# Kernel tuning notes

Hardware: AMD Instinct MI355X
Metric: run time of the kernel (lower is better)

Reference implementation:

```python
import jax, jax.numpy as jnp
import numpy as np

N = 50000
E = 800000
IN_CH = 256
HID = 32
HEADS = 4
OUT_CH = 40
NEG_SLOPE = 0.2
BN_EPS = 1e-5


def _gat_conv(x, W, att_src, att_dst, bias, src, dst, num_nodes, concat):
    # x: [N, F_in]; W: [F_in, H*C]; att_src/att_dst: [H, C]
    H, C = att_src.shape
    h = (x @ W).reshape(num_nodes, H, C)            # [N, H, C]
    a_src = (h * att_src[None]).sum(-1)             # [N, H]
    a_dst = (h * att_dst[None]).sum(-1)             # [N, H]
    e = jax.nn.leaky_relu(a_src[src] + a_dst[dst], NEG_SLOPE)  # [Etot, H]
    # segment softmax over incoming edges of each destination node
    m = jax.ops.segment_max(e, dst, num_segments=num_nodes)    # [N, H]
    ex = jnp.exp(e - m[dst])
    s = jax.ops.segment_sum(ex, dst, num_segments=num_nodes)   # [N, H]
    alpha = ex / (s[dst] + 1e-16)                   # [Etot, H]
    out = jax.ops.segment_sum(h[src] * alpha[:, :, None], dst,
                              num_segments=num_nodes)          # [N, H, C]
    out = out.reshape(num_nodes, H * C) if concat else out.mean(axis=1)
    return out + bias


def setup_inputs() -> dict:
    key = jax.random.key(0)
    ks = jax.random.split(key, 12)
    x = jax.random.normal(ks[0], (N, IN_CH), dtype=jnp.float32)
    edge_index = jax.random.randint(ks[1], (2, E), 0, N, dtype=jnp.int64)
    # layer 1: in -> heads*hid, concat
    W1 = jax.random.normal(ks[2], (IN_CH, HEADS * HID), dtype=jnp.float32) * (1.0 / np.sqrt(IN_CH))
    att_src1 = jax.random.normal(ks[3], (HEADS, HID), dtype=jnp.float32) * 0.1
    att_dst1 = jax.random.normal(ks[4], (HEADS, HID), dtype=jnp.float32) * 0.1
    b1 = jnp.zeros((HEADS * HID,), dtype=jnp.float32)
    # batch norm over hidden*heads features
    gamma = jnp.ones((HEADS * HID,), dtype=jnp.float32)
    beta = jnp.zeros((HEADS * HID,), dtype=jnp.float32)
    # layer 2: heads*hid -> out, heads=1, mean (concat=False)
    W2 = jax.random.normal(ks[5], (HEADS * HID, OUT_CH), dtype=jnp.float32) * (1.0 / np.sqrt(HEADS * HID))
    att_src2 = jax.random.normal(ks[6], (1, OUT_CH), dtype=jnp.float32) * 0.1
    att_dst2 = jax.random.normal(ks[7], (1, OUT_CH), dtype=jnp.float32) * 0.1
    b2 = jnp.zeros((OUT_CH,), dtype=jnp.float32)
    return {"x": x, "edge_index": edge_index, "W1": W1, "att_src1": att_src1,
            "att_dst1": att_dst1, "b1": b1, "gamma": gamma, "beta": beta,
            "W2": W2, "att_src2": att_src2, "att_dst2": att_dst2, "b2": b2}


def reference(x, edge_index, W1, att_src1, att_dst1, b1, gamma, beta,
              W2, att_src2, att_dst2, b2):
    num_nodes = x.shape[0]
    loops = jnp.arange(num_nodes, dtype=edge_index.dtype)
    src = jnp.concatenate([edge_index[0], loops])   # add self-loops (PyG default)
    dst = jnp.concatenate([edge_index[1], loops])
    h = _gat_conv(x, W1, att_src1, att_dst1, b1, src, dst, num_nodes, concat=True)
    # BatchNorm over nodes (training-mode batch statistics)
    mu = h.mean(axis=0)
    var = h.var(axis=0)
    h = (h - mu) * jax.lax.rsqrt(var + BN_EPS) * gamma + beta
    h = jax.nn.elu(h)
    out = _gat_conv(h, W2, att_src2, att_dst2, b2, src, dst, num_nodes, concat=False)
    return out
```

## Files before the change

### kernel.cpp

```cpp
#include <hip/hip_runtime.h>

#define NN 50000
#define EE 800000
#define FIN 256
#define F1 128
#define F2 40
#define CAP 48
#define G1B ((NN + 63) / 64)
#define FILLB ((EE + 255) / 256)
#define G1PB 3126
#define G2P0 3125
#define G2P1 ((NN + 63) / 64)
#define LSTR 56

typedef unsigned int u32;
typedef unsigned short u16;
typedef _Float16 h8 __attribute__((ext_vector_type(8)));
typedef float f4 __attribute__((ext_vector_type(4)));

static __device__ __forceinline__ u32 f2bf(float f) {
  u32 u = __float_as_uint(f);
  return (u + 0x7FFFu + ((u >> 16) & 1u)) >> 16;
}
#define BF_LO(u) __uint_as_float((u) << 16)
#define BF_HI(u) __uint_as_float((u) & 0xFFFF0000u)

__global__ __launch_bounds__(256) void g1f_kernel(const float* __restrict__ x,
                                                  const float* __restrict__ W1,
                                                  const float* __restrict__ att_src,
                                                  const float* __restrict__ att_dst,
                                                  u32* __restrict__ h1bf,
                                                  float* __restrict__ a_src,
                                                  float* __restrict__ a_dst,
                                                  const int* __restrict__ ei,
                                                  int* __restrict__ cnt,
                                                  u16* __restrict__ csr) {
  __shared__ __align__(16) _Float16 Alds[64 * LSTR];
  __shared__ __align__(16) _Float16 Blds[128 * LSTR];
  const int t = threadIdx.x;

  if (blockIdx.x >= G1B) {
    int e = (blockIdx.x - G1B) * 256 + t;
    if (e < EE) {
      int src = ei[e];
      int dst = ei[EE + e];
      int p = atomicAdd(cnt + dst, 1);
      if (p < CAP) csr[dst * CAP + p] = (u16)src;
    }
    return;
  }

  const int m0 = blockIdx.x * 64;
  const int l  = t & 63;
  const int w  = t >> 6;
  const int q  = l & 15;
  const int hq = l >> 4;

  const int arow  = t >> 2;
  const int akoff = (t & 3) * 8;
  const int bn    = t & 127;
  const int bkh   = (t >> 7) * 16;

  f4 acc[8] = {};

  float ax[8];
  float bx[16];
  {
    int gr = m0 + arow;
    if (gr < NN) {
      float4 u0 = *(const float4*)(x + (size_t)gr * FIN + akoff);
      float4 u1 = *(const float4*)(x + (size_t)gr * FIN + akoff + 4);
      ax[0] = u0.x; ax[1] = u0.y; ax[2] = u0.z; ax[3] = u0.w;
      ax[4] = u1.x; ax[5] = u1.y; ax[6] = u1.z; ax[7] = u1.w;
    } else {
#pragma unroll
      for (int i = 0; i < 8; ++i) ax[i] = 0.f;
    }
#pragma unroll
    for (int i = 0; i < 16; ++i) bx[i] = W1[(size_t)(bkh + i) * F1 + bn];
  }

  for (int s = 0; s < 8; ++s) {
    __syncthreads();
    {
      h8 av;
#pragma unroll
      for (int i = 0; i < 8; ++i) av[i] = (_Float16)ax[i];
      *(h8*)(Alds + arow * LSTR + akoff) = av;
      h8 bv0, bv1;
#pragma unroll
      for (int i = 0; i < 8; ++i) { bv0[i] = (_Float16)bx[i]; bv1[i] = (_Float16)bx[8 + i]; }
      *(h8*)(Blds + bn * LSTR + bkh) = bv0;
      *(h8*)(Blds + bn * LSTR + bkh + 8) = bv1;
    }
    __syncthreads();
    if (s < 7) {
      int k0 = (s + 1) * 32;
      int gr = m0 + arow;
      if (gr < NN) {
        float4 u0 = *(const float4*)(x + (size_t)gr * FIN + k0 + akoff);
        float4 u1 = *(const float4*)(x + (size_t)gr * FIN + k0 + akoff + 4);
        ax[0] = u0.x; ax[1] = u0.y; ax[2] = u0.z; ax[3] = u0.w;
        ax[4] = u1.x; ax[5] = u1.y; ax[6] = u1.z; ax[7] = u1.w;
      } else {
#pragma unroll
        for (int i = 0; i < 8; ++i) ax[i] = 0.f;
      }
#pragma unroll
      for (int i = 0; i < 16; ++i) bx[i] = W1[(size_t)(k0 + bkh + i) * F1 + bn];
    }
    h8 af = *(const h8*)(Alds + (w * 16 + q) * LSTR + hq * 8);
#pragma unroll
    for (int nf = 0; nf < 8; ++nf) {
      h8 bf = *(const h8*)(Blds + (nf * 16 + q) * LSTR + hq * 8);
      acc[nf] = __builtin_amdgcn_mfma_f32_16x16x32_f16(af, bf, acc[nf], 0, 0, 0);
    }
  }

  u16* h1u = (u16*)h1bf;
#pragma unroll
  for (int nf = 0; nf < 8; ++nf) {
    int ph = nf >> 1;
#pragma unroll
    for (int r = 0; r < 4; ++r) {
      int grow = m0 + w * 16 + hq * 4 + r;
      if (grow < NN)
        h1u[((size_t)ph * NN + grow) * 32 + (nf & 1) * 16 + q] = (u16)f2bf(acc[nf][r]);
    }
  }
  float as8[8], ad8[8];
#pragma unroll
  for (int nf = 0; nf < 8; ++nf) {
    as8[nf] = att_src[nf * 16 + q];
    ad8[nf] = att_dst[nf * 16 + q];
  }
#pragma unroll
  for (int r = 0; r < 4; ++r) {
    float p0 = acc[0][r] * as8[0] + acc[1][r] * as8[1];
    float p1 = acc[2][r] * as8[2] + acc[3][r] * as8[3];
    float p2 = acc[4][r] * as8[4] + acc[5][r] * as8[5];
    float p3 = acc[6][r] * as8[6] + acc[7][r] * as8[7];
    float d0 = acc[0][r] * ad8[0] + acc[1][r] * ad8[1];
    float d1 = acc[2][r] * ad8[2] + acc[3][r] * ad8[3];
    float d2 = acc[4][r] * ad8[4] + acc[5][r] * ad8[5];
    float d3 = acc[6][r] * ad8[6] + acc[7][r] * ad8[7];
#pragma unroll
    for (int off = 1; off < 16; off <<= 1) {
      p0 += __shfl_xor(p0, off); p1 += __shfl_xor(p1, off);
      p2 += __shfl_xor(p2, off); p3 += __shfl_xor(p3, off);
      d0 += __shfl_xor(d0, off); d1 += __shfl_xor(d1, off);
      d2 += __shfl_xor(d2, off); d3 += __shfl_xor(d3, off);
    }
    int grow = m0 + w * 16 + hq * 4 + r;
    if (grow < NN && q < 8) {
      float vs = (q & 2) ? ((q & 1) ? p3 : p2) : ((q & 1) ? p1 : p0);
      float vd = (q & 2) ? ((q & 1) ? d3 : d2) : ((q & 1) ? d1 : d0);
      if (q < 4) a_src[grow * 4 + q] = vs;
      else       a_dst[grow * 4 + (q - 4)] = vd;
    }
  }
}

__global__ __launch_bounds__(256) void gather1_kernel(const int* __restrict__ cnt,
                                                      const u16* __restrict__ csr,
                                                      const float* __restrict__ a_src,
                                                      const float* __restrict__ a_dst,
                                                      const u32* __restrict__ h1bf,
                                                      const float* __restrict__ b1,
                                                      float* __restrict__ h1b,
                                                      float* __restrict__ bnsum,
                                                      float* __restrict__ bnsq) {
  __shared__ float bns[32], bnq[32];
  int t = threadIdx.x;
  if (t < 32) { bns[t] = 0.f; bnq[t] = 0.f; }
  __syncthreads();
  int d = blockIdx.x;
  int xcd = d & 7;
  int p = xcd >> 1;
  int nb = ((d >> 3) << 1) + (xcd & 1);
  int n = nb * 16 + (t >> 4);
  int sub = t & 15;
  int g = sub >> 2;
  int l = sub & 3;
  int f0 = p * 32 + l * 8;
  float acc[8] = {0.f, 0.f, 0.f, 0.f, 0.f, 0.f, 0.f, 0.f};
  float ssum = 0.f;
  if (n < NN) {
    float adst = a_dst[n * 4 + p];
    const u32* hb = h1bf + (size_t)p * NN * 16 + l * 4;
    if (g == 0) {
      float e0 = a_src[n * 4 + p] + adst;
      e0 = e0 > 0.f ? e0 : 0.2f * e0;
      float x0 = __expf(e0);
      uint4 qv = *(const uint4*)(hb + (size_t)n * 16);
      acc[0] = fmaf(x0, BF_LO(qv.x), acc[0]); acc[1] = fmaf(x0, BF_HI(qv.x), acc[1]);
      acc[2] = fmaf(x0, BF_LO(qv.y), acc[2]); acc[3] = fmaf(x0, BF_HI(qv.y), acc[3]);
      acc[4] = fmaf(x0, BF_LO(qv.z), acc[4]); acc[5] = fmaf(x0, BF_HI(qv.z), acc[5]);
      acc[6] = fmaf(x0, BF_LO(qv.w), acc[6]); acc[7] = fmaf(x0, BF_HI(qv.w), acc[7]);
      ssum += x0;
    }
    const u16* row = csr + (size_t)n * CAP;
    int m = cnt[n]; if (m > CAP) m = CAP;
    int i = g;
    for (; i + 4 < m; i += 8) {
      int s0 = row[i];
      int s1 = row[i + 4];
      float e0 = a_src[s0 * 4 + p];
      float e1 = a_src[s1 * 4 + p];
      uint4 q0 = *(const uint4*)(hb + (size_t)s0 * 16);
      uint4 q1 = *(const uint4*)(hb + (size_t)s1 * 16);
      e0 += adst; e0 = e0 > 0.f ? e0 : 0.2f * e0;  float x0 = __expf(e0);
      e1 += adst; e1 = e1 > 0.f ? e1 : 0.2f * e1;  float x1 = __expf(e1);
      acc[0] = fmaf(x0, BF_LO(q0.x), acc[0]); acc[1] = fmaf(x0, BF_HI(q0.x), acc[1]);
      acc[2] = fmaf(x0, BF_LO(q0.y), acc[2]); acc[3] = fmaf(x0, BF_HI(q0.y), acc[3]);
      acc[4] = fmaf(x0, BF_LO(q0.z), acc[4]); acc[5] = fmaf(x0, BF_HI(q0.z), acc[5]);
      acc[6] = fmaf(x0, BF_LO(q0.w), acc[6]); acc[7] = fmaf(x0, BF_HI(q0.w), acc[7]);
      acc[0] = fmaf(x1, BF_LO(q1.x), acc[0]); acc[1] = fmaf(x1, BF_HI(q1.x), acc[1]);
      acc[2] = fmaf(x1, BF_LO(q1.y), acc[2]); acc[3] = fmaf(x1, BF_HI(q1.y), acc[3]);
      acc[4] = fmaf(x1, BF_LO(q1.z), acc[4]); acc[5] = fmaf(x1, BF_HI(q1.z), acc[5]);
      acc[6] = fmaf(x1, BF_LO(q1.w), acc[6]); acc[7] = fmaf(x1, BF_HI(q1.w), acc[7]);
      ssum += x0 + x1;
    }
    for (; i < m; i += 4) {
      int s0 = row[i];
      float e0 = a_src[s0 * 4 + p] + adst;
      e0 = e0 > 0.f ? e0 : 0.2f * e0;
      float x0 = __expf(e0);
      uint4 qv = *(const uint4*)(hb + (size_t)s0 * 16);
      acc[0] = fmaf(x0, BF_LO(qv.x), acc[0]); acc[1] = fmaf(x0, BF_HI(qv.x), acc[1]);
      acc[2] = fmaf(x0, BF_LO(qv.y), acc[2]); acc[3] = fmaf(x0, BF_HI(qv.y), acc[3]);
      acc[4] = fmaf(x0, BF_LO(qv.z), acc[4]); acc[5] = fmaf(x0, BF_HI(qv.z), acc[5]);
      acc[6] = fmaf(x0, BF_LO(qv.w), acc[6]); acc[7] = fmaf(x0, BF_HI(qv.w), acc[7]);
      ssum += x0;
    }
  }
#pragma unroll
  for (int j = 0; j < 8; ++j) {
    acc[j] += __shfl_xor(acc[j], 4);
    acc[j] += __shfl_xor(acc[j], 8);
  }
  ssum += __shfl_xor(ssum, 4);
  ssum += __shfl_xor(ssum, 8);
  if (n < NN && g == 0) {
    float inv = 1.f / (ssum + 1e-16f);
    float4 b0 = *(const float4*)(b1 + f0);
    float4 b4 = *(const float4*)(b1 + f0 + 4);
    float o[8];
    o[0] = acc[0] * inv + b0.x; o[1] = acc[1] * inv + b0.y;
    o[2] = acc[2] * inv + b0.z; o[3] = acc[3] * inv + b0.w;
    o[4] = acc[4] * inv + b4.x; o[5] = acc[5] * inv + b4.y;
    o[6] = acc[6] * inv + b4.z; o[7] = acc[7] * inv + b4.w;
    float4 w0 = {o[0], o[1], o[2], o[3]};
    float4 w1 = {o[4], o[5], o[6], o[7]};
    *(float4*)(h1b + (size_t)n * F1 + f0) = w0;
    *(float4*)(h1b + (size_t)n * F1 + f0 + 4) = w1;
    int lb = l * 8;
#pragma unroll
    for (int j = 0; j < 8; ++j) {
      atomicAdd(&bns[lb + j], o[j]);
      atomicAdd(&bnq[lb + j], o[j] * o[j]);
    }
  }
  __syncthreads();
  if (t < 32) {
    atomicAdd(bnsum + p * 32 + t, bns[t]);
    atomicAdd(bnsq + p * 32 + t, bnq[t]);
  }
}

__global__ __launch_bounds__(256) void gemm2_kernel(const float* __restrict__ hpre,
                                                    const float* __restrict__ W2,
                                                    const float* __restrict__ bnsum,
                                                    const float* __restrict__ bnsq,
                                                    const float* __restrict__ gamma,
                                                    const float* __restrict__ beta,
                                                    u16* __restrict__ h2a,
                                                    u16* __restrict__ h2b,
                                                    const float* __restrict__ att_src2,
                                                    const float* __restrict__ att_dst2,
                                                    float* __restrict__ a_src2,
                                                    float* __restrict__ a_dst2) {
  __shared__ float Wlds[128 * 40];
  __shared__ float Alds[16 * 128];
  __shared__ float sc[128], sh[128];
  int t = threadIdx.x;
  for (int i = t; i < 128 * 40; i += 256) Wlds[i] = W2[i];
  if (t < 128) {
    const float invN = 1.f / (float)NN;
    float mu = bnsum[t] * invN;
    float var = bnsq[t] * invN - mu * mu;
    float s = gamma[t] * rsqrtf(var + 1e-5f);
    sc[t] = s;
    sh[t] = beta[t] - mu * s;
  }
  int tr = t >> 3;
  int tc = t & 7;
  float as5[5], ad5[5];
#pragma unroll
  for (int j = 0; j < 5; ++j) { as5[j] = att_src2[tc * 5 + j]; ad5[j] = att_dst2[tc * 5 + j]; }
  int n0 = blockIdx.x * 128;
  int lrow = t >> 1;
  int lkk = (t & 1) * 8;
  float acc[4][5];
#pragma unroll
  for (int i = 0; i < 4; ++i)
#pragma unroll
    for (int j = 0; j < 5; ++j) acc[i][j] = 0.f;

  for (int k0 = 0; k0 < F1; k0 += 16) {
    float av[8];
    int gn = n0 + lrow;
    if (gn < NN) {
      float4 v0 = *(const float4*)(hpre + (size_t)gn * F1 + k0 + lkk);
      float4 v1 = *(const float4*)(hpre + (size_t)gn * F1 + k0 + lkk + 4);
      av[0] = v0.x; av[1] = v0.y; av[2] = v0.z; av[3] = v0.w;
      av[4] = v1.x; av[5] = v1.y; av[6] = v1.z; av[7] = v1.w;
    } else {
#pragma unroll
      for (int j = 0; j < 8; ++j) av[j] = 0.f;
    }
    __syncthreads();
#pragma unroll
    for (int j = 0; j < 8; ++j) {
      int kg = k0 + lkk + j;
      float a = av[j] * sc[kg] + sh[kg];
      a = a > 0.f ? a : (__expf(a) - 1.f);
      Alds[(lkk + j) * 128 + lrow] = a;
    }
    __syncthreads();
#pragma unroll
    for (int k = 0; k < 16; ++k) {
      float4 a4 = *(const float4*)(Alds + k * 128 + tr * 4);
      float aa[4] = {a4.x, a4.y, a4.z, a4.w};
      float w[5];
#pragma unroll
      for (int j = 0; j < 5; ++j) w[j] = Wlds[(k0 + k) * 40 + tc * 5 + j];
#pragma unroll
      for (int i = 0; i < 4; ++i)
#pragma unroll
        for (int j = 0; j < 5; ++j) acc[i][j] = fmaf(aa[i], w[j], acc[i][j]);
    }
  }
#pragma unroll
  for (int i = 0; i < 4; ++i) {
    int gn = n0 + tr * 4 + i;
    if (gn < NN) {
#pragma unroll
      for (int j = 0; j < 5; ++j) {
        int f = tc * 5 + j;
        u16 v = (u16)f2bf(acc[i][j]);
        if (f < 32) h2a[(size_t)gn * 32 + f] = v;
        else        h2b[(size_t)gn * 8 + (f - 32)] = v;
      }
    }
  }
#pragma unroll
  for (int i = 0; i < 4; ++i) {
    float ps = 0.f, pd = 0.f;
#pragma unroll
    for (int j = 0; j < 5; ++j) { ps += acc[i][j] * as5[j]; pd += acc[i][j] * ad5[j]; }
#pragma unroll
    for (int off = 1; off < 8; off <<= 1) {
      ps += __shfl_xor(ps, off);
      pd += __shfl_xor(pd, off);
    }
    if (tc == 0) {
      int gn = n0 + tr * 4 + i;
      if (gn < NN) { a_src2[gn] = ps; a_dst2[gn] = pd; }
    }
  }
}

__global__ __launch_bounds__(256) void gather2_kernel(const int* __restrict__ cnt,
                                                      const u16* __restrict__ csr,
                                                      const float* __restrict__ a_src,
                                                      const float* __restrict__ a_dst,
                                                      const u32* __restrict__ h2a,
                                                      const u32* __restrict__ h2b,
                                                      const float* __restrict__ b2,
                                                      float* __restrict__ out) {
  int t = threadIdx.x;
  int d = blockIdx.x;
  if (d < G2P0) {
    int n = d * 16 + (t >> 4);
    int sub = t & 15;
    int g = sub >> 2;
    int l = sub & 3;
    float adst = a_dst[n];
    const u32* hb = h2a + l * 4;
    float acc[8] = {0.f, 0.f, 0.f, 0.f, 0.f, 0.f, 0.f, 0.f};
    float ssum = 0.f;
    if (g == 0) {
      float e0 = a_src[n] + adst;
      e0 = e0 > 0.f ? e0 : 0.2f * e0;
      float x0 = __expf(e0);
      uint4 qv = *(const uint4*)(hb + (size_t)n * 16);
      acc[0] = fmaf(x0, BF_LO(qv.x), acc[0]); acc[1] = fmaf(x0, BF_HI(qv.x), acc[1]);
      acc[2] = fmaf(x0, BF_LO(qv.y), acc[2]); acc[3] = fmaf(x0, BF_HI(qv.y), acc[3]);
      acc[4] = fmaf(x0, BF_LO(qv.z), acc[4]); acc[5] = fmaf(x0, BF_HI(qv.z), acc[5]);
      acc[6] = fmaf(x0, BF_LO(qv.w), acc[6]); acc[7] = fmaf(x0, BF_HI(qv.w), acc[7]);
      ssum += x0;
    }
    const u16* row = csr + (size_t)n * CAP;
    int m = cnt[n]; if (m > CAP) m = CAP;
    int i = g;
    for (; i + 4 < m; i += 8) {
      int s0 = row[i];
      int s1 = row[i + 4];
      float e0 = a_src[s0];
      float e1 = a_src[s1];
      uint4 q0 = *(const uint4*)(hb + (size_t)s0 * 16);
      uint4 q1 = *(const uint4*)(hb + (size_t)s1 * 16);
      e0 += adst; e0 = e0 > 0.f ? e0 : 0.2f * e0;  float x0 = __expf(e0);
      e1 += adst; e1 = e1 > 0.f ? e1 : 0.2f * e1;  float x1 = __expf(e1);
      acc[0] = fmaf(x0, BF_LO(q0.x), acc[0]); acc[1] = fmaf(x0, BF_HI(q0.x), acc[1]);
      acc[2] = fmaf(x0, BF_LO(q0.y), acc[2]); acc[3] = fmaf(x0, BF_HI(q0.y), acc[3]);
      acc[4] = fmaf(x0, BF_LO(q0.z), acc[4]); acc[5] = fmaf(x0, BF_HI(q0.z), acc[5]);
      acc[6] = fmaf(x0, BF_LO(q0.w), acc[6]); acc[7] = fmaf(x0, BF_HI(q0.w), acc[7]);
      acc[0] = fmaf(x1, BF_LO(q1.x), acc[0]); acc[1] = fmaf(x1, BF_HI(q1.x), acc[1]);
      acc[2] = fmaf(x1, BF_LO(q1.y), acc[2]); acc[3] = fmaf(x1, BF_HI(q1.y), acc[3]);
      acc[4] = fmaf(x1, BF_LO(q1.z), acc[4]); acc[5] = fmaf(x1, BF_HI(q1.z), acc[5]);
      acc[6] = fmaf(x1, BF_LO(q1.w), acc[6]); acc[7] = fmaf(x1, BF_HI(q1.w), acc[7]);
      ssum += x0 + x1;
    }
    for (; i < m; i += 4) {
      int s0 = row[i];
      float e0 = a_src[s0] + adst;
      e0 = e0 > 0.f ? e0 : 0.2f * e0;
      float x0 = __expf(e0);
      uint4 qv = *(const uint4*)(hb + (size_t)s0 * 16);
      acc[0] = fmaf(x0, BF_LO(qv.x), acc[0]); acc[1] = fmaf(x0, BF_HI(qv.x), acc[1]);
      acc[2] = fmaf(x0, BF_LO(qv.y), acc[2]); acc[3] = fmaf(x0, BF_HI(qv.y), acc[3]);
      acc[4] = fmaf(x0, BF_LO(qv.z), acc[4]); acc[5] = fmaf(x0, BF_HI(qv.z), acc[5]);
      acc[6] = fmaf(x0, BF_LO(qv.w), acc[6]); acc[7] = fmaf(x0, BF_HI(qv.w), acc[7]);
      ssum += x0;
    }
#pragma unroll
    for (int j = 0; j < 8; ++j) {
      acc[j] += __shfl_xor(acc[j], 4);
      acc[j] += __shfl_xor(acc[j], 8);
    }
    ssum += __shfl_xor(ssum, 4);
    ssum += __shfl_xor(ssum, 8);
    if (g == 0) {
      float inv = 1.f / (ssum + 1e-16f);
      int f0 = l * 8;
      float4 b0 = *(const float4*)(b2 + f0);
      float4 b4 = *(const float4*)(b2 + f0 + 4);
      float4 w0 = {acc[0] * inv + b0.x, acc[1] * inv + b0.y,
                   acc[2] * inv + b0.z, acc[3] * inv + b0.w};
      float4 w1 = {acc[4] * inv + b4.x, acc[5] * inv + b4.y,
                   acc[6] * inv + b4.z, acc[7] * inv + b4.w};
      *(float4*)(out + (size_t)n * F2 + f0) = w0;
      *(float4*)(out + (size_t)n * F2 + f0 + 4) = w1;
    }
  } else {
    int n = (d - G2P0) * 64 + (t >> 2);
    int g = t & 3;
    float acc[8] = {0.f, 0.f, 0.f, 0.f, 0.f, 0.f, 0.f, 0.f};
    float ssum = 0.f;
    if (n < NN) {
      float adst = a_dst[n];
      if (g == 0) {
        float e0 = a_src[n] + adst;
        e0 = e0 > 0.f ? e0 : 0.2f * e0;
        float x0 = __expf(e0);
        uint4 qv = *(const uint4*)(h2b + (size_t)n * 4);
        acc[0] = fmaf(x0, BF_LO(qv.x), acc[0]); acc[1] = fmaf(x0, BF_HI(qv.x), acc[1]);
        acc[2] = fmaf(x0, BF_LO(qv.y), acc[2]); acc[3] = fmaf(x0, BF_HI(qv.y), acc[3]);
        acc[4] = fmaf(x0, BF_LO(qv.z), acc[4]); acc[5] = fmaf(x0, BF_HI(qv.z), acc[5]);
        acc[6] = fmaf(x0, BF_LO(qv.w), acc[6]); acc[7] = fmaf(x0, BF_HI(qv.w), acc[7]);
        ssum += x0;
      }
      const u16* row = csr + (size_t)n * CAP;
      int m = cnt[n]; if (m > CAP) m = CAP;
      int i = g;
      for (; i + 4 < m; i += 8) {
        int s0 = row[i];
        int s1 = row[i + 4];
        float e0 = a_src[s0];
        float e1 = a_src[s1];
        uint4 q0 = *(const uint4*)(h2b + (size_t)s0 * 4);
        uint4 q1 = *(const uint4*)(h2b + (size_t)s1 * 4);
        e0 += adst; e0 = e0 > 0.f ? e0 : 0.2f * e0;  float x0 = __expf(e0);
        e1 += adst; e1 = e1 > 0.f ? e1 : 0.2f * e1;  float x1 = __expf(e1);
        acc[0] = fmaf(x0, BF_LO(q0.x), acc[0]); acc[1] = fmaf(x0, BF_HI(q0.x), acc[1]);
        acc[2] = fmaf(x0, BF_LO(q0.y), acc[2]); acc[3] = fmaf(x0, BF_HI(q0.y), acc[3]);
        acc[4] = fmaf(x0, BF_LO(q0.z), acc[4]); acc[5] = fmaf(x0, BF_HI(q0.z), acc[5]);
        acc[6] = fmaf(x0, BF_LO(q0.w), acc[6]); acc[7] = fmaf(x0, BF_HI(q0.w), acc[7]);
        acc[0] = fmaf(x1, BF_LO(q1.x), acc[0]); acc[1] = fmaf(x1, BF_HI(q1.x), acc[1]);
        acc[2] = fmaf(x1, BF_LO(q1.y), acc[2]); acc[3] = fmaf(x1, BF_HI(q1.y), acc[3]);
        acc[4] = fmaf(x1, BF_LO(q1.z), acc[4]); acc[5] = fmaf(x1, BF_HI(q1.z), acc[5]);
        acc[6] = fmaf(x1, BF_LO(q1.w), acc[6]); acc[7] = fmaf(x1, BF_HI(q1.w), acc[7]);
        ssum += x0 + x1;
      }
      for (; i < m; i += 4) {
        int s0 = row[i];
        float e0 = a_src[s0] + adst;
        e0 = e0 > 0.f ? e0 : 0.2f * e0;
        float x0 = __expf(e0);
        uint4 qv = *(const uint4*)(h2b + (size_t)s0 * 4);
        acc[0] = fmaf(x0, BF_LO(qv.x), acc[0]); acc[1] = fmaf(x0, BF_HI(qv.x), acc[1]);
        acc[2] = fmaf(x0, BF_LO(qv.y), acc[2]); acc[3] = fmaf(x0, BF_HI(qv.y), acc[3]);
        acc[4] = fmaf(x0, BF_LO(qv.z), acc[4]); acc[5] = fmaf(x0, BF_HI(qv.z), acc[5]);
        acc[6] = fmaf(x0, BF_LO(qv.w), acc[6]); acc[7] = fmaf(x0, BF_HI(qv.w), acc[7]);
        ssum += x0;
      }
    }
#pragma unroll
    for (int j = 0; j < 8; ++j) {
      acc[j] += __shfl_xor(acc[j], 1);
      acc[j] += __shfl_xor(acc[j], 2);
    }
    ssum += __shfl_xor(ssum, 1);
    ssum += __shfl_xor(ssum, 2);
    if (n < NN && g == 0) {
      float inv = 1.f / (ssum + 1e-16f);
      float4 b0 = *(const float4*)(b2 + 32);
      float4 b4 = *(const float4*)(b2 + 36);
      float4 w0 = {acc[0] * inv + b0.x, acc[1] * inv + b0.y,
                   acc[2] * inv + b0.z, acc[3] * inv + b0.w};
      float4 w1 = {acc[4] * inv + b4.x, acc[5] * inv + b4.y,
                   acc[6] * inv + b4.z, acc[7] * inv + b4.w};
      *(float4*)(out + (size_t)n * F2 + 32) = w0;
      *(float4*)(out + (size_t)n * F2 + 36) = w1;
    }
  }
}

extern "C" void kernel_launch(void* const* d_in, const int* in_sizes, int n_in,
                              void* d_out, int out_size, void* d_ws, size_t ws_size,
                              hipStream_t stream) {
  const float* x        = (const float*)d_in[0];
  const int*   ei       = (const int*)d_in[1];
  const float* W1       = (const float*)d_in[2];
  const float* att_src1 = (const float*)d_in[3];
  const float* att_dst1 = (const float*)d_in[4];
  const float* b1       = (const float*)d_in[5];
  const float* gamma    = (const float*)d_in[6];
  const float* beta     = (const float*)d_in[7];
  const float* W2       = (const float*)d_in[8];
  const float* att_src2 = (const float*)d_in[9];
  const float* att_dst2 = (const float*)d_in[10];
  const float* b2       = (const float*)d_in[11];
  float* out = (float*)d_out;

  int* cnt      = (int*)d_ws;
  float* bnsum  = (float*)(cnt + 50048);
  float* bnsq   = bnsum + 128;
  u16* csr      = (u16*)(bnsq + 128);
  u32* h1bf     = (u32*)(csr + (size_t)NN * CAP);
  float* h1b    = (float*)(h1bf + 3200000);
  u32* h2a      = (u32*)(h1b + 6400000);
  u32* h2b      = h2a + 800000;
  float* a_src1 = (float*)(h2b + 200000);
  float* a_dst1 = a_src1 + 200000;
  float* a_src2 = a_dst1 + 200000;
  float* a_dst2 = a_src2 + 50000;

  hipMemsetAsync(cnt, 0, (50048 + 256) * sizeof(int), stream);

  g1f_kernel<<<G1B + FILLB, 256, 0, stream>>>(x, W1, att_src1, att_dst1,
                                              h1bf, a_src1, a_dst1,
                                              ei, cnt, csr);
  gather1_kernel<<<(G1PB / 2) * 8, 256, 0, stream>>>(cnt, csr, a_src1, a_dst1,
                                                     h1bf, b1, h1b, bnsum, bnsq);
  gemm2_kernel<<<(NN + 127) / 128, 256, 0, stream>>>(h1b, W2, bnsum, bnsq,
                                                     gamma, beta,
                                                     (u16*)h2a, (u16*)h2b,
                                                     att_src2, att_dst2,
                                                     a_src2, a_dst2);
  gather2_kernel<<<G2P0 + G2P1, 256, 0, stream>>>(cnt, csr, a_src2, a_dst2,
                                                  h2a, h2b, b2, out);
}
```

Baseline: 290.2 us.

## Stage CSR rows in LDS and split edges contiguously with shuffled attention loads

```diff
diff --git a/kernel.cpp b/kernel.cpp
--- a/kernel.cpp
+++ b/kernel.cpp
@@ -24,6 +24,12 @@
 }
 #define BF_LO(u) __uint_as_float((u) << 16)
 #define BF_HI(u) __uint_as_float((u) & 0xFFFF0000u)
+
+static __device__ __forceinline__ int sel4i(int a, int b, int c, int d, int k) {
+  int lo = (k & 1) ? b : a;
+  int hi = (k & 1) ? d : c;
+  return (k & 2) ? hi : lo;
+}
 
 __global__ __launch_bounds__(256) void g1f_kernel(const float* __restrict__ x,
                                                   const float* __restrict__ W1,
@@ -171,21 +177,26 @@
                                                       float* __restrict__ bnsum,
                                                       float* __restrict__ bnsq) {
   __shared__ float bns[32], bnq[32];
+  __shared__ __align__(16) u16 idx[16 * CAP];
   int t = threadIdx.x;
   if (t < 32) { bns[t] = 0.f; bnq[t] = 0.f; }
-  __syncthreads();
   int d = blockIdx.x;
   int xcd = d & 7;
   int p = xcd >> 1;
   int nb = ((d >> 3) << 1) + (xcd & 1);
-  int n = nb * 16 + (t >> 4);
+  int base_n = nb * 16;
+  bool blk_ok = (nb < 3125);
+  if (blk_ok && t < 96)
+    ((uint4*)idx)[t] = ((const uint4*)(csr + (size_t)base_n * CAP))[t];
+  __syncthreads();
+  int n = base_n + (t >> 4);
   int sub = t & 15;
   int g = sub >> 2;
   int l = sub & 3;
   int f0 = p * 32 + l * 8;
   float acc[8] = {0.f, 0.f, 0.f, 0.f, 0.f, 0.f, 0.f, 0.f};
   float ssum = 0.f;
-  if (n < NN) {
+  if (blk_ok) {
     float adst = a_dst[n * 4 + p];
     const u32* hb = h1bf + (size_t)p * NN * 16 + l * 4;
     if (g == 0) {
@@ -199,18 +210,30 @@
       acc[6] = fmaf(x0, BF_LO(qv.w), acc[6]); acc[7] = fmaf(x0, BF_HI(qv.w), acc[7]);
       ssum += x0;
     }
-    const u16* row = csr + (size_t)n * CAP;
+    const u16* lrow = idx + (t >> 4) * CAP;
     int m = cnt[n]; if (m > CAP) m = CAP;
-    int i = g;
-    for (; i + 4 < m; i += 8) {
-      int s0 = row[i];
-      int s1 = row[i + 4];
-      float e0 = a_src[s0 * 4 + p];
-      float e1 = a_src[s1 * 4 + p];
+    int sp = (m + 3) >> 2;
+    int i = g * sp;
+    int end = i + sp; if (end > m) end = m;
+    int gb = (t & 63) & ~3;
+    for (; i + 3 < end; i += 4) {
+      int s0 = lrow[i + 0];
+      int s1 = lrow[i + 1];
+      int s2 = lrow[i + 2];
+      int s3 = lrow[i + 3];
+      float av = a_src[sel4i(s0, s1, s2, s3, l) * 4 + p];
       uint4 q0 = *(const uint4*)(hb + (size_t)s0 * 16);
       uint4 q1 = *(const uint4*)(hb + (size_t)s1 * 16);
-      e0 += adst; e0 = e0 > 0.f ? e0 : 0.2f * e0;  float x0 = __expf(e0);
-      e1 += adst; e1 = e1 > 0.f ? e1 : 0.2f * e1;  float x1 = __expf(e1);
+      uint4 q2 = *(const uint4*)(hb + (size_t)s2 * 16);
+      uint4 q3 = *(const uint4*)(hb + (size_t)s3 * 16);
+      float e0 = __shfl(av, gb + 0, 64) + adst;
+      float e1 = __shfl(av, gb + 1, 64) + adst;
+      float e2 = __shfl(av, gb + 2, 64) + adst;
+      float e3 = __shfl(av, gb + 3, 64) + adst;
+      e0 = e0 > 0.f ? e0 : 0.2f * e0;  float x0 = __expf(e0);
+      e1 = e1 > 0.f ? e1 : 0.2f * e1;  float x1 = __expf(e1);
+      e2 = e2 > 0.f ? e2 : 0.2f * e2;  float x2 = __expf(e2);
+      e3 = e3 > 0.f ? e3 : 0.2f * e3;  float x3 = __expf(e3);
       acc[0] = fmaf(x0, BF_LO(q0.x), acc[0]); acc[1] = fmaf(x0, BF_HI(q0.x), acc[1]);
       acc[2] = fmaf(x0, BF_LO(q0.y), acc[2]); acc[3] = fmaf(x0, BF_HI(q0.y), acc[3]);
       acc[4] = fmaf(x0, BF_LO(q0.z), acc[4]); acc[5] = fmaf(x0, BF_HI(q0.z), acc[5]);
@@ -219,10 +242,18 @@
       acc[2] = fmaf(x1, BF_LO(q1.y), acc[2]); acc[3] = fmaf(x1, BF_HI(q1.y), acc[3]);
       acc[4] = fmaf(x1, BF_LO(q1.z), acc[4]); acc[5] = fmaf(x1, BF_HI(q1.z), acc[5]);
       acc[6] = fmaf(x1, BF_LO(q1.w), acc[6]); acc[7] = fmaf(x1, BF_HI(q1.w), acc[7]);
-      ssum += x0 + x1;
-    }
-    for (; i < m; i += 4) {
-      int s0 = row[i];
+      acc[0] = fmaf(x2, BF_LO(q2.x), acc[0]); acc[1] = fmaf(x2, BF_HI(q2.x), acc[1]);
+      acc[2] = fmaf(x2, BF_LO(q2.y), acc[2]); acc[3] = fmaf(x2, BF_HI(q2.y), acc[3]);
+      acc[4] = fmaf(x2, BF_LO(q2.z), acc[4]); acc[5] = fmaf(x2, BF_HI(q2.z), acc[5]);
+      acc[6] = fmaf(x2, BF_LO(q2.w), acc[6]); acc[7] = fmaf(x2, BF_HI(q2.w), acc[7]);
+      acc[0] = fmaf(x3, BF_LO(q3.x), acc[0]); acc[1] = fmaf(x3, BF_HI(q3.x), acc[1]);
+      acc[2] = fmaf(x3, BF_LO(q3.y), acc[2]); acc[3] = fmaf(x3, BF_HI(q3.y), acc[3]);
+      acc[4] = fmaf(x3, BF_LO(q3.z), acc[4]); acc[5] = fmaf(x3, BF_HI(q3.z), acc[5]);
+      acc[6] = fmaf(x3, BF_LO(q3.w), acc[6]); acc[7] = fmaf(x3, BF_HI(q3.w), acc[7]);
+      ssum += x0 + x1 + x2 + x3;
+    }
+    for (; i < end; ++i) {
+      int s0 = lrow[i];
       float e0 = a_src[s0 * 4 + p] + adst;
       e0 = e0 > 0.f ? e0 : 0.2f * e0;
       float x0 = __expf(e0);
@@ -241,7 +272,7 @@
   }
   ssum += __shfl_xor(ssum, 4);
   ssum += __shfl_xor(ssum, 8);
-  if (n < NN && g == 0) {
+  if (blk_ok && g == 0) {
     float inv = 1.f / (ssum + 1e-16f);
     float4 b0 = *(const float4*)(b1 + f0);
     float4 b4 = *(const float4*)(b1 + f0 + 4);
@@ -382,7 +413,12 @@
   int t = threadIdx.x;
   int d = blockIdx.x;
   if (d < G2P0) {
-    int n = d * 16 + (t >> 4);
+    __shared__ __align__(16) u16 idx[16 * CAP];
+    int base_n = d * 16;
+    if (t < 96)
+      ((uint4*)idx)[t] = ((const uint4*)(csr + (size_t)base_n * CAP))[t];
+    __syncthreads();
+    int n = base_n + (t >> 4);
     int sub = t & 15;
     int g = sub >> 2;
     int l = sub & 3;
@@ -401,18 +437,30 @@
       acc[6] = fmaf(x0, BF_LO(qv.w), acc[6]); acc[7] = fmaf(x0, BF_HI(qv.w), acc[7]);
       ssum += x0;
     }
-    const u16* row = csr + (size_t)n * CAP;
+    const u16* lrow = idx + (t >> 4) * CAP;
     int m = cnt[n]; if (m > CAP) m = CAP;
-    int i = g;
-    for (; i + 4 < m; i += 8) {
-      int s0 = row[i];
-      int s1 = row[i + 4];
-      float e0 = a_src[s0];
-      float e1 = a_src[s1];
+    int sp = (m + 3) >> 2;
+    int i = g * sp;
+    int end = i + sp; if (end > m) end = m;
+    int gb = (t & 63) & ~3;
+    for (; i + 3 < end; i += 4) {
+      int s0 = lrow[i + 0];
+      int s1 = lrow[i + 1];
+      int s2 = lrow[i + 2];
+      int s3 = lrow[i + 3];
+      float av = a_src[sel4i(s0, s1, s2, s3, l)];
       uint4 q0 = *(const uint4*)(hb + (size_t)s0 * 16);
       uint4 q1 = *(const uint4*)(hb + (size_t)s1 * 16);
-      e0 += adst; e0 = e0 > 0.f ? e0 : 0.2f * e0;  float x0 = __expf(e0);
-      e1 += adst; e1 = e1 > 0.f ? e1 : 0.2f * e1;  float x1 = __expf(e1);
+      uint4 q2 = *(const uint4*)(hb + (size_t)s2 * 16);
+      uint4 q3 = *(const uint4*)(hb + (size_t)s3 * 16);
+      float e0 = __shfl(av, gb + 0, 64) + adst;
+      float e1 = __shfl(av, gb + 1, 64) + adst;
+      float e2 = __shfl(av, gb + 2, 64) + adst;
+      float e3 = __shfl(av, gb + 3, 64) + adst;
+      e0 = e0 > 0.f ? e0 : 0.2f * e0;  float x0 = __expf(e0);
+      e1 = e1 > 0.f ? e1 : 0.2f * e1;  float x1 = __expf(e1);
+      e2 = e2 > 0.f ? e2 : 0.2f * e2;  float x2 = __expf(e2);
+      e3 = e3 > 0.f ? e3 : 0.2f * e3;  float x3 = __expf(e3);
       acc[0] = fmaf(x0, BF_LO(q0.x), acc[0]); acc[1] = fmaf(x0, BF_HI(q0.x), acc[1]);
       acc[2] = fmaf(x0, BF_LO(q0.y), acc[2]); acc[3] = fmaf(x0, BF_HI(q0.y), acc[3]);
       acc[4] = fmaf(x0, BF_LO(q0.z), acc[4]); acc[5] = fmaf(x0, BF_HI(q0.z), acc[5]);
@@ -421,10 +469,18 @@
       acc[2] = fmaf(x1, BF_LO(q1.y), acc[2]); acc[3] = fmaf(x1, BF_HI(q1.y), acc[3]);
       acc[4] = fmaf(x1, BF_LO(q1.z), acc[4]); acc[5] = fmaf(x1, BF_HI(q1.z), acc[5]);
       acc[6] = fmaf(x1, BF_LO(q1.w), acc[6]); acc[7] = fmaf(x1, BF_HI(q1.w), acc[7]);
-      ssum += x0 + x1;
-    }
-    for (; i < m; i += 4) {
-      int s0 = row[i];
+      acc[0] = fmaf(x2, BF_LO(q2.x), acc[0]); acc[1] = fmaf(x2, BF_HI(q2.x), acc[1]);
+      acc[2] = fmaf(x2, BF_LO(q2.y), acc[2]); acc[3] = fmaf(x2, BF_HI(q2.y), acc[3]);
+      acc[4] = fmaf(x2, BF_LO(q2.z), acc[4]); acc[5] = fmaf(x2, BF_HI(q2.z), acc[5]);
+      acc[6] = fmaf(x2, BF_LO(q2.w), acc[6]); acc[7] = fmaf(x2, BF_HI(q2.w), acc[7]);
+      acc[0] = fmaf(x3, BF_LO(q3.x), acc[0]); acc[1] = fmaf(x3, BF_HI(q3.x), acc[1]);
+      acc[2] = fmaf(x3, BF_LO(q3.y), acc[2]); acc[3] = fmaf(x3, BF_HI(q3.y), acc[3]);
+      acc[4] = fmaf(x3, BF_LO(q3.z), acc[4]); acc[5] = fmaf(x3, BF_HI(q3.z), acc[5]);
+      acc[6] = fmaf(x3, BF_LO(q3.w), acc[6]); acc[7] = fmaf(x3, BF_HI(q3.w), acc[7]);
+      ssum += x0 + x1 + x2 + x3;
+    }
+    for (; i < end; ++i) {
+      int s0 = lrow[i];
       float e0 = a_src[s0] + adst;
       e0 = e0 > 0.f ? e0 : 0.2f * e0;
       float x0 = __expf(e0);
```

After: 287.8 us. Within noise of the previous version (-0.8%).
